# Kernel optimization log

Measured on AMD Instinct MI355X. Metric: run time of the kernel, lower is better.

The kernel has to match this reference:

```python
import jax, jax.numpy as jnp
import numpy as np

DIM = 512
GLBL = 108
N = 100000
NUM_SEGMENTS = 1024


def setup_inputs() -> dict:
    key = jax.random.key(0)
    ks = jax.random.split(key, 9)
    x = jax.random.normal(ks[0], (N, DIM), dtype=jnp.float32)
    glbl_x = jax.random.normal(ks[1], (N, GLBL), dtype=jnp.float32)
    batch = jnp.sort(jax.random.randint(ks[2], (N,), 0, NUM_SEGMENTS, dtype=jnp.int32))
    # MLP params: (dim+108 -> dim), (dim -> dim), (dim -> 1)
    s0 = 1.0 / np.sqrt(DIM + GLBL)
    s1 = 1.0 / np.sqrt(DIM)
    W0 = jax.random.uniform(ks[3], (DIM + GLBL, DIM), jnp.float32, -s0, s0)
    b0 = jax.random.uniform(ks[4], (DIM,), jnp.float32, -s0, s0)
    W1 = jax.random.uniform(ks[5], (DIM, DIM), jnp.float32, -s1, s1)
    b1 = jax.random.uniform(ks[6], (DIM,), jnp.float32, -s1, s1)
    W2 = jax.random.uniform(ks[7], (DIM, 1), jnp.float32, -s1, s1)
    b2 = jax.random.uniform(ks[8], (1,), jnp.float32, -s1, s1)
    return {"x": x, "batch": batch, "glbl_x": glbl_x,
            "W0": W0, "b0": b0, "W1": W1, "b1": b1, "W2": W2, "b2": b2}


def segment_softmax(logits, seg, num_segments):
    # logits: [N, 1]; per-segment numerically-stable softmax (torch_geometric softmax)
    m = jax.ops.segment_max(logits, seg, num_segments=num_segments)  # [G, 1]
    e = jnp.exp(logits - m[seg])
    s = jax.ops.segment_sum(e, seg, num_segments=num_segments)       # [G, 1]
    return e / (s[seg] + 1e-16)


def reference(x, batch, glbl_x, W0, b0, W1, b1, W2, b2):
    out = jnp.concatenate([x, glbl_x], axis=-1)          # [N, dim+108]
    out = jax.nn.softplus(out @ W0 + b0)                 # [N, dim]
    out = jax.nn.softplus(out @ W1 + b1)                 # [N, dim]
    out = out @ W2 + b2                                  # [N, 1]
    return segment_softmax(out, batch, NUM_SEGMENTS)     # [N, 1]
```

## Files before the change

kernel.cpp:

```cpp
#include <hip/hip_runtime.h>
#include <hip/hip_bf16.h>
#include <math.h>


#define NSEG 1024

typedef __attribute__((ext_vector_type(8))) short short8;
typedef __attribute__((ext_vector_type(4))) float f32x4;

__device__ __forceinline__ unsigned short f2bf(float f) {
  __hip_bfloat16 h = __float2bfloat16(f);
  return *reinterpret_cast<unsigned short*>(&h);
}
__device__ __forceinline__ float softplus_fast(float z) {
  float t = __expf(-fabsf(z));
  return fmaxf(z, 0.f) + __logf(1.f + t);
}
__device__ __forceinline__ void gll16(const unsigned short* g, unsigned short* l) {
  __builtin_amdgcn_global_load_lds(
      (const __attribute__((address_space(1))) void*)g,
      (__attribute__((address_space(3))) void*)l, 16, 0, 0);
}
__device__ __forceinline__ int xcd_swz(int bid, int nwg) {
  int q = nwg >> 3, r = nwg & 7, x = bid & 7, i = bid >> 3;
  return (x < r ? x * (q + 1) : r * (q + 1) + (x - r) * q) + i;
}

__global__ __launch_bounds__(256) void prep(const float* __restrict__ W0,
                                            const float* __restrict__ W1,
                                            unsigned short* __restrict__ W0T,
                                            unsigned short* __restrict__ W1T,
                                            float* __restrict__ logits, int Mp) {
  int t = blockIdx.x * 256 + threadIdx.x;
  if (t < 512 * 640) {
    int n = t / 640, k = t % 640;
    W0T[t] = f2bf(k < 620 ? W0[(size_t)k * 512 + n] : 0.f);
    return;
  }
  t -= 512 * 640;
  if (t < 512 * 512) {
    int n = t / 512, k = t % 512;
    W1T[t] = f2bf(W1[(size_t)k * 512 + n]);
    return;
  }
  t -= 512 * 512;
  if (t < Mp) logits[t] = 0.f;
}

__global__ __launch_bounds__(256, 3) void gemm0(const float* __restrict__ x,
                                                const float* __restrict__ gx,
                                                const unsigned short* __restrict__ W0T,
                                                const float* __restrict__ b0,
                                                unsigned short* __restrict__ H0,
                                                int N, int nwg) {
  constexpr int K = 640, KT = 20;
  __shared__ unsigned short As[2][128 * 32];
  __shared__ unsigned short Ws[2][128 * 32];
  const int L = xcd_swz(blockIdx.x, nwg);
  const int nt = L & 3, mt = L >> 2;
  const int tid = threadIdx.x, lane = tid & 63, wid = tid >> 6;
  const int wm = wid >> 1, wn = wid & 1, lm = lane & 15, rch = lane >> 4;

  const int arow_l = tid >> 1, ah = tid & 1;
  const int arow_g = mt * 128 + arow_l;
  const int ap = (arow_l >> 1) & 3;
  const bool avalid = arow_g < N;
  const unsigned short* Wg = W0T + (size_t)(nt * 128) * K;

  f32x4 acc[4][4] = {};
  float4 va[4];

  auto loadA = [&](int kt) {
    const int c0 = kt * 32 + ah * 16;
    if (kt < 16) {
      if (avalid) {
        const float4* p = (const float4*)(x + (size_t)arow_g * 512 + c0);
#pragma unroll
        for (int j = 0; j < 4; ++j) va[j] = p[j];
      } else {
#pragma unroll
        for (int j = 0; j < 4; ++j) va[j] = float4{0.f, 0.f, 0.f, 0.f};
      }
    } else {
      const int g0 = c0 - 512;
      float tmp[16];
#pragma unroll
      for (int j = 0; j < 16; ++j) {
        int col = g0 + j;
        tmp[j] = (avalid && col < 108) ? gx[(size_t)arow_g * 108 + col] : 0.f;
      }
#pragma unroll
      for (int j = 0; j < 4; ++j)
        va[j] = float4{tmp[4 * j], tmp[4 * j + 1], tmp[4 * j + 2], tmp[4 * j + 3]};
    }
  };
  auto writeA = [&](int buf) {
    union { unsigned short u[8]; uint4 qv; } w0, w1;
    w0.u[0] = f2bf(va[0].x); w0.u[1] = f2bf(va[0].y); w0.u[2] = f2bf(va[0].z); w0.u[3] = f2bf(va[0].w);
    w0.u[4] = f2bf(va[1].x); w0.u[5] = f2bf(va[1].y); w0.u[6] = f2bf(va[1].z); w0.u[7] = f2bf(va[1].w);
    w1.u[0] = f2bf(va[2].x); w1.u[1] = f2bf(va[2].y); w1.u[2] = f2bf(va[2].z); w1.u[3] = f2bf(va[2].w);
    w1.u[4] = f2bf(va[3].x); w1.u[5] = f2bf(va[3].y); w1.u[6] = f2bf(va[3].z); w1.u[7] = f2bf(va[3].w);
    const int s0 = (2 * ah) ^ ap, s1 = (2 * ah + 1) ^ ap;
    *reinterpret_cast<uint4*>(&As[buf][arow_l * 32 + s0 * 8]) = w0.qv;
    *reinterpret_cast<uint4*>(&As[buf][arow_l * 32 + s1 * 8]) = w1.qv;
  };
  auto stageW = [&](int buf, int kb) {
#pragma unroll
    for (int i2 = 0; i2 < 2; ++i2) {
      int f = i2 * 256 + tid;
      int row = f >> 2;
      int sc = ((f & 3) ^ ((row >> 1) & 3)) << 3;
      gll16(Wg + (size_t)row * K + kb + sc, &Ws[buf][f * 8]);
    }
  };

  stageW(0, 0);
  loadA(0);
  writeA(0);
  loadA(1);

  for (int kt = 0; kt < KT; ++kt) {
    const int cur = kt & 1;
    __syncthreads();
    if (kt + 1 < KT) {
      stageW(cur ^ 1, (kt + 1) * 32);
      writeA(cur ^ 1);
    }
    if (kt + 2 < KT) loadA(kt + 2);

    short8 af[4], wf[4];
#pragma unroll
    for (int mi = 0; mi < 4; ++mi) {
      int rw = wm * 64 + mi * 16 + lm;
      af[mi] = *reinterpret_cast<const short8*>(
          &As[cur][rw * 32 + ((rch ^ ((rw >> 1) & 3)) << 3)]);
    }
#pragma unroll
    for (int ni = 0; ni < 4; ++ni) {
      int rw = wn * 64 + ni * 16 + lm;
      wf[ni] = *reinterpret_cast<const short8*>(
          &Ws[cur][rw * 32 + ((rch ^ ((rw >> 1) & 3)) << 3)]);
    }
    __builtin_amdgcn_s_setprio(1);
#pragma unroll
    for (int mi = 0; mi < 4; ++mi)
#pragma unroll
      for (int ni = 0; ni < 4; ++ni)
        acc[mi][ni] = __builtin_amdgcn_mfma_f32_16x16x32_bf16(wf[ni], af[mi], acc[mi][ni], 0, 0, 0);
    __builtin_amdgcn_s_setprio(0);
  }

#pragma unroll
  for (int mi = 0; mi < 4; ++mi) {
    const int m = mt * 128 + wm * 64 + mi * 16 + lm;
#pragma unroll
    for (int ni = 0; ni < 4; ++ni) {
      const int n0 = nt * 128 + wn * 64 + ni * 16 + (rch << 2);
      const f32x4 bb = *reinterpret_cast<const f32x4*>(b0 + n0);
      f32x4 v = acc[mi][ni];
      union { unsigned short u[4]; uint2 qv; } o;
#pragma unroll
      for (int rr = 0; rr < 4; ++rr) o.u[rr] = f2bf(softplus_fast(v[rr] + bb[rr]));
      *reinterpret_cast<uint2*>(H0 + (size_t)m * 512 + n0) = o.qv;
    }
  }
}

__global__ __launch_bounds__(256, 3) void gemm1(const unsigned short* __restrict__ H0,
                                                const unsigned short* __restrict__ W1T,
                                                const float* __restrict__ b1,
                                                const float* __restrict__ W2,
                                                float* __restrict__ logits, int nwg) {
  constexpr int K = 512, KT = 16;
  __shared__ unsigned short As[2][128 * 32];
  __shared__ unsigned short Ws[2][128 * 32];
  const int L = xcd_swz(blockIdx.x, nwg);
  const int nt = L & 3, mt = L >> 2;
  const int tid = threadIdx.x, lane = tid & 63, wid = tid >> 6;
  const int wm = wid >> 1, wn = wid & 1, lm = lane & 15, rch = lane >> 4;

  const unsigned short* Ag = H0 + (size_t)(mt * 128) * K;
  const unsigned short* Wg = W1T + (size_t)(nt * 128) * K;

  f32x4 acc[4][4] = {};

  auto stage = [&](int buf, int kb) {
#pragma unroll
    for (int i2 = 0; i2 < 2; ++i2) {
      int f = i2 * 256 + tid;
      int row = f >> 2;
      int sc = ((f & 3) ^ ((row >> 1) & 3)) << 3;
      gll16(Ag + (size_t)row * K + kb + sc, &As[buf][f * 8]);
      gll16(Wg + (size_t)row * K + kb + sc, &Ws[buf][f * 8]);
    }
  };

  stage(0, 0);

  for (int kt = 0; kt < KT; ++kt) {
    const int cur = kt & 1;
    __syncthreads();
    if (kt + 1 < KT) stage(cur ^ 1, (kt + 1) * 32);

    short8 af[4], wf[4];
#pragma unroll
    for (int mi = 0; mi < 4; ++mi) {
      int rw = wm * 64 + mi * 16 + lm;
      af[mi] = *reinterpret_cast<const short8*>(
          &As[cur][rw * 32 + ((rch ^ ((rw >> 1) & 3)) << 3)]);
    }
#pragma unroll
    for (int ni = 0; ni < 4; ++ni) {
      int rw = wn * 64 + ni * 16 + lm;
      wf[ni] = *reinterpret_cast<const short8*>(
          &Ws[cur][rw * 32 + ((rch ^ ((rw >> 1) & 3)) << 3)]);
    }
    __builtin_amdgcn_s_setprio(1);
#pragma unroll
    for (int mi = 0; mi < 4; ++mi)
#pragma unroll
      for (int ni = 0; ni < 4; ++ni)
        acc[mi][ni] = __builtin_amdgcn_mfma_f32_16x16x32_bf16(wf[ni], af[mi], acc[mi][ni], 0, 0, 0);
    __builtin_amdgcn_s_setprio(0);
  }

#pragma unroll
  for (int mi = 0; mi < 4; ++mi) {
    const int m = mt * 128 + wm * 64 + mi * 16 + lm;
    float part = 0.f;
#pragma unroll
    for (int ni = 0; ni < 4; ++ni) {
      const int n0 = nt * 128 + wn * 64 + ni * 16 + (rch << 2);
      const f32x4 bb = *reinterpret_cast<const f32x4*>(b1 + n0);
      const f32x4 wv = *reinterpret_cast<const f32x4*>(W2 + n0);
      f32x4 v = acc[mi][ni];
#pragma unroll
      for (int rr = 0; rr < 4; ++rr) part += softplus_fast(v[rr] + bb[rr]) * wv[rr];
    }
    part += __shfl_xor(part, 16);
    part += __shfl_xor(part, 32);
    if (lane < 16) atomicAdd(logits + m, part);
  }
}

__global__ __launch_bounds__(256) void segsoftmax(const float* __restrict__ logits,
                                                  const int* __restrict__ batch,
                                                  float* __restrict__ out, int N) {
  const int g = blockIdx.x;
  const int tid = threadIdx.x;
  int lo = 0, hi = N;
  while (lo < hi) { int mid = (lo + hi) >> 1; if (batch[mid] < g) lo = mid + 1; else hi = mid; }
  const int beg = lo;
  hi = N;
  while (lo < hi) { int mid = (lo + hi) >> 1; if (batch[mid] < g + 1) lo = mid + 1; else hi = mid; }
  const int end = lo;
  if (beg >= end) return;

  __shared__ float sh[4];
  float m = -INFINITY;
  for (int i = beg + tid; i < end; i += 256) m = fmaxf(m, logits[i]);
#pragma unroll
  for (int o = 32; o; o >>= 1) m = fmaxf(m, __shfl_down(m, o));
  if ((tid & 63) == 0) sh[tid >> 6] = m;
  __syncthreads();
  m = fmaxf(fmaxf(sh[0], sh[1]), fmaxf(sh[2], sh[3]));
  __syncthreads();

  float s = 0.f;
  for (int i = beg + tid; i < end; i += 256) s += expf(logits[i] - m);
#pragma unroll
  for (int o = 32; o; o >>= 1) s += __shfl_down(s, o);
  if ((tid & 63) == 0) sh[tid >> 6] = s;
  __syncthreads();
  s = sh[0] + sh[1] + sh[2] + sh[3];

  const float inv = 1.f / (s + 1e-16f);
  for (int i = beg + tid; i < end; i += 256) out[i] = expf(logits[i] - m) * inv;
}

extern "C" void kernel_launch(void* const* d_in, const int* in_sizes, int n_in,
                              void* d_out, int out_size, void* d_ws, size_t ws_size,
                              hipStream_t stream) {
  const float* x = (const float*)d_in[0];
  const int* batch = (const int*)d_in[1];
  const float* gx = (const float*)d_in[2];
  const float* W0 = (const float*)d_in[3];
  const float* b0 = (const float*)d_in[4];
  const float* W1 = (const float*)d_in[5];
  const float* b1 = (const float*)d_in[6];
  const float* W2 = (const float*)d_in[7];
  float* out = (float*)d_out;

  const int N = in_sizes[1];
  const int Mp = ((N + 127) / 128) * 128;
  const int nwg = (Mp / 128) * 4;

  auto align256 = [](size_t v) { return (v + 255) & ~(size_t)255; };
  char* ws = (char*)d_ws;
  size_t off = 0;
  unsigned short* W0T = (unsigned short*)(ws + off); off = align256(off + (size_t)512 * 640 * 2);
  unsigned short* W1T = (unsigned short*)(ws + off); off = align256(off + (size_t)512 * 512 * 2);
  unsigned short* H0 = (unsigned short*)(ws + off);  off = align256(off + (size_t)Mp * 512 * 2);
  float* logits = (float*)(ws + off);                off = align256(off + (size_t)Mp * 4);
  (void)ws_size; (void)n_in; (void)out_size;

  const int prep_elems = 512 * 640 + 512 * 512 + Mp;
  prep<<<(prep_elems + 255) / 256, 256, 0, stream>>>(W0, W1, W0T, W1T, logits, Mp);

  gemm0<<<nwg, 256, 0, stream>>>(x, gx, W0T, b0, H0, N, nwg);
  gemm1<<<nwg, 256, 0, stream>>>(H0, W1T, b1, W2, logits, nwg);

  segsoftmax<<<NSEG, 256, 0, stream>>>(logits, batch, out, N);
}
```

Measured before the change: 315.1 us.

## Stage fp32 activations via direct global-to-LDS loads and pre-pad glbl_x

The activation operand of the first GEMM is now loaded straight into LDS as fp32 with global_load_lds instead of going through registers, and is converted to bf16 when fragments are read from LDS. A new pack kernel copies glbl_x into a 128-column, zero-padded, 16-byte-aligned buffer so those direct loads also work for the glbl_x columns. The second GEMM's launch bounds move from 3 to 4 waves per SIMD. The cost is double the LDS per A tile, a bf16 conversion repeated by every wave that reads a fragment, and an extra kernel launch plus pass over glbl_x.

```diff
diff --git a/kernel.cpp b/kernel.cpp
--- a/kernel.cpp
+++ b/kernel.cpp
@@ -16,7 +16,7 @@
   float t = __expf(-fabsf(z));
   return fmaxf(z, 0.f) + __logf(1.f + t);
 }
-__device__ __forceinline__ void gll16(const unsigned short* g, unsigned short* l) {
+__device__ __forceinline__ void gll16(const void* g, void* l) {
   __builtin_amdgcn_global_load_lds(
       (const __attribute__((address_space(1))) void*)g,
       (__attribute__((address_space(3))) void*)l, 16, 0, 0);
@@ -47,62 +47,54 @@
   if (t < Mp) logits[t] = 0.f;
 }
 
+__global__ __launch_bounds__(256) void pack_g(const float* __restrict__ gx,
+                                              float* __restrict__ G32,
+                                              int N, int Mp) {
+  int t = blockIdx.x * 256 + threadIdx.x;
+  if (t >= Mp * 32) return;
+  int row = t >> 5, c = (t & 31) << 2;
+  float4 v;
+  v.x = (row < N && c + 0 < 108) ? gx[(size_t)row * 108 + c + 0] : 0.f;
+  v.y = (row < N && c + 1 < 108) ? gx[(size_t)row * 108 + c + 1] : 0.f;
+  v.z = (row < N && c + 2 < 108) ? gx[(size_t)row * 108 + c + 2] : 0.f;
+  v.w = (row < N && c + 3 < 108) ? gx[(size_t)row * 108 + c + 3] : 0.f;
+  *reinterpret_cast<float4*>(G32 + (size_t)row * 128 + c) = v;
+}
+
 __global__ __launch_bounds__(256, 3) void gemm0(const float* __restrict__ x,
-                                                const float* __restrict__ gx,
+                                                const float* __restrict__ G32,
                                                 const unsigned short* __restrict__ W0T,
                                                 const float* __restrict__ b0,
                                                 unsigned short* __restrict__ H0,
                                                 int N, int nwg) {
   constexpr int K = 640, KT = 20;
-  __shared__ unsigned short As[2][128 * 32];
+  __shared__ float Asf[2][128 * 32];
   __shared__ unsigned short Ws[2][128 * 32];
   const int L = xcd_swz(blockIdx.x, nwg);
   const int nt = L & 3, mt = L >> 2;
   const int tid = threadIdx.x, lane = tid & 63, wid = tid >> 6;
   const int wm = wid >> 1, wn = wid & 1, lm = lane & 15, rch = lane >> 4;
 
-  const int arow_l = tid >> 1, ah = tid & 1;
-  const int arow_g = mt * 128 + arow_l;
-  const int ap = (arow_l >> 1) & 3;
-  const bool avalid = arow_g < N;
   const unsigned short* Wg = W0T + (size_t)(nt * 128) * K;
 
   f32x4 acc[4][4] = {};
-  float4 va[4];
-
-  auto loadA = [&](int kt) {
-    const int c0 = kt * 32 + ah * 16;
-    if (kt < 16) {
-      if (avalid) {
-        const float4* p = (const float4*)(x + (size_t)arow_g * 512 + c0);
-#pragma unroll
-        for (int j = 0; j < 4; ++j) va[j] = p[j];
+
+  auto stageA = [&](int buf, int kb) {
+#pragma unroll
+    for (int i2 = 0; i2 < 4; ++i2) {
+      int f = i2 * 256 + tid;
+      int r = f >> 3, s = f & 7;
+      int g4 = (s ^ (r & 7)) << 2;
+      const float* src;
+      if (kb < 512) {
+        int rg = mt * 128 + r; if (rg >= N) rg = N - 1;
+        src = x + (size_t)rg * 512 + kb + g4;
       } else {
-#pragma unroll
-        for (int j = 0; j < 4; ++j) va[j] = float4{0.f, 0.f, 0.f, 0.f};
+        int rg = mt * 128 + r;
+        src = G32 + (size_t)rg * 128 + (kb - 512) + g4;
       }
-    } else {
-      const int g0 = c0 - 512;
-      float tmp[16];
-#pragma unroll
-      for (int j = 0; j < 16; ++j) {
-        int col = g0 + j;
-        tmp[j] = (avalid && col < 108) ? gx[(size_t)arow_g * 108 + col] : 0.f;
-      }
-#pragma unroll
-      for (int j = 0; j < 4; ++j)
-        va[j] = float4{tmp[4 * j], tmp[4 * j + 1], tmp[4 * j + 2], tmp[4 * j + 3]};
-    }
-  };
-  auto writeA = [&](int buf) {
-    union { unsigned short u[8]; uint4 qv; } w0, w1;
-    w0.u[0] = f2bf(va[0].x); w0.u[1] = f2bf(va[0].y); w0.u[2] = f2bf(va[0].z); w0.u[3] = f2bf(va[0].w);
-    w0.u[4] = f2bf(va[1].x); w0.u[5] = f2bf(va[1].y); w0.u[6] = f2bf(va[1].z); w0.u[7] = f2bf(va[1].w);
-    w1.u[0] = f2bf(va[2].x); w1.u[1] = f2bf(va[2].y); w1.u[2] = f2bf(va[2].z); w1.u[3] = f2bf(va[2].w);
-    w1.u[4] = f2bf(va[3].x); w1.u[5] = f2bf(va[3].y); w1.u[6] = f2bf(va[3].z); w1.u[7] = f2bf(va[3].w);
-    const int s0 = (2 * ah) ^ ap, s1 = (2 * ah + 1) ^ ap;
-    *reinterpret_cast<uint4*>(&As[buf][arow_l * 32 + s0 * 8]) = w0.qv;
-    *reinterpret_cast<uint4*>(&As[buf][arow_l * 32 + s1 * 8]) = w1.qv;
+      gll16(src, &Asf[buf][r * 32 + s * 4]);
+    }
   };
   auto stageW = [&](int buf, int kb) {
 #pragma unroll
@@ -114,26 +106,25 @@
     }
   };
 
+  stageA(0, 0);
   stageW(0, 0);
-  loadA(0);
-  writeA(0);
-  loadA(1);
 
   for (int kt = 0; kt < KT; ++kt) {
     const int cur = kt & 1;
     __syncthreads();
-    if (kt + 1 < KT) {
-      stageW(cur ^ 1, (kt + 1) * 32);
-      writeA(cur ^ 1);
-    }
-    if (kt + 2 < KT) loadA(kt + 2);
+    if (kt + 1 < KT) { stageA(cur ^ 1, (kt + 1) * 32); stageW(cur ^ 1, (kt + 1) * 32); }
 
     short8 af[4], wf[4];
 #pragma unroll
     for (int mi = 0; mi < 4; ++mi) {
       int rw = wm * 64 + mi * 16 + lm;
-      af[mi] = *reinterpret_cast<const short8*>(
-          &As[cur][rw * 32 + ((rch ^ ((rw >> 1) & 3)) << 3)]);
+      const float* base = &Asf[cur][rw * 32];
+      f32x4 lo = *reinterpret_cast<const f32x4*>(base + ((((2 * rch) ^ (rw & 7)) << 2)));
+      f32x4 hi = *reinterpret_cast<const f32x4*>(base + ((((2 * rch + 1) ^ (rw & 7)) << 2)));
+      union { unsigned short u[8]; short8 s8; } cv;
+#pragma unroll
+      for (int j = 0; j < 4; ++j) { cv.u[j] = f2bf(lo[j]); cv.u[4 + j] = f2bf(hi[j]); }
+      af[mi] = cv.s8;
     }
 #pragma unroll
     for (int ni = 0; ni < 4; ++ni) {
@@ -166,7 +157,7 @@
   }
 }
 
-__global__ __launch_bounds__(256, 3) void gemm1(const unsigned short* __restrict__ H0,
+__global__ __launch_bounds__(256, 4) void gemm1(const unsigned short* __restrict__ H0,
                                                 const unsigned short* __restrict__ W1T,
                                                 const float* __restrict__ b1,
                                                 const float* __restrict__ W2,
@@ -298,6 +289,7 @@
   auto align256 = [](size_t v) { return (v + 255) & ~(size_t)255; };
   char* ws = (char*)d_ws;
   size_t off = 0;
+  float* G32 = (float*)(ws + off);                   off = align256(off + (size_t)Mp * 128 * 4);
   unsigned short* W0T = (unsigned short*)(ws + off); off = align256(off + (size_t)512 * 640 * 2);
   unsigned short* W1T = (unsigned short*)(ws + off); off = align256(off + (size_t)512 * 512 * 2);
   unsigned short* H0 = (unsigned short*)(ws + off);  off = align256(off + (size_t)Mp * 512 * 2);
@@ -306,8 +298,9 @@
 
   const int prep_elems = 512 * 640 + 512 * 512 + Mp;
   prep<<<(prep_elems + 255) / 256, 256, 0, stream>>>(W0, W1, W0T, W1T, logits, Mp);
-
-  gemm0<<<nwg, 256, 0, stream>>>(x, gx, W0T, b0, H0, N, nwg);
+  pack_g<<<(Mp * 32 + 255) / 256, 256, 0, stream>>>(gx, G32, N, Mp);
+
+  gemm0<<<nwg, 256, 0, stream>>>(x, G32, W0T, b0, H0, N, nwg);
   gemm1<<<nwg, 256, 0, stream>>>(H0, W1T, b1, W2, logits, nwg);
 
   segsoftmax<<<NSEG, 256, 0, stream>>>(logits, batch, out, N);
```

New measurement: 273.2 us. -13.3%, faster.
